# Kernel optimization log

Measured on AMD Instinct MI355X. Metric: run time of the kernel, lower is better.

Reference implementation:

```python
import jax, jax.numpy as jnp
import numpy as np
from jax import lax

T, H, K, V, O = 8192, 2048, 512, 512, 2048


def setup_inputs() -> dict:
    key = jax.random.key(0)
    ks = jax.random.split(key, 11)
    s_h = 1.0 / np.sqrt(H)
    s_v = 1.0 / np.sqrt(V)
    return {
        "hidden_state": jax.random.normal(ks[0], (T, H), jnp.float32),
        "Wq": jax.random.normal(ks[1], (H, K), jnp.float32) * s_h,
        "bq": jax.random.normal(ks[2], (K,), jnp.float32) * 0.02,
        "Wk": jax.random.normal(ks[3], (H, K), jnp.float32) * s_h,
        "bk": jax.random.normal(ks[4], (K,), jnp.float32) * 0.02,
        "Wv": jax.random.normal(ks[5], (H, V), jnp.float32) * s_h,
        "bv": jax.random.normal(ks[6], (V,), jnp.float32) * 0.02,
        "Wg": jax.random.normal(ks[7], (H, K), jnp.float32) * s_h,
        "bg": jax.random.normal(ks[8], (K,), jnp.float32) * 0.02,
        "Wo": jax.random.normal(ks[9], (V, O), jnp.float32) * s_v,
        "bo": jax.random.normal(ks[10], (O,), jnp.float32) * 0.02,
    }


def reference(hidden_state, Wq, bq, Wk, bk, Wv, bv, Wg, bg, Wo, bo):
    # Batched projections (torch Linear: x @ W^T + b; here W stored as [in,out])
    q = hidden_state @ Wq + bq                    # [T, K]
    k = jax.nn.sigmoid(hidden_state @ Wk + bk)    # [T, K]
    g = jax.nn.sigmoid(hidden_state @ Wg + bg)    # [T, K]
    v = hidden_state @ Wv + bv                    # [T, V]

    def step(state, qkvg):
        qi, ki, vi, gi = qkvg
        # state: [K, V]; gated decay per key-dim row, then outer-product write
        state = state * gi[:, None] + ki[:, None] * vi[None, :]
        out_i = qi @ state  # == state.T @ qi -> [V]
        return state, out_i

    init = jnp.zeros((K, V), hidden_state.dtype)
    final_state, outs = lax.scan(step, init, (q, k, v, g))  # outs: [T, V]
    output = outs @ Wo + bo                                  # [T, O]
    return output, final_state
```

## Files before the change

### kernel.cpp

```cpp
#include <hip/hip_runtime.h>

#define T_LEN 8192
#define H_DIM 2048
#define K_DIM 512
#define V_DIM 512
#define O_DIM 2048
#define CHUNK 64
#define NCHUNK 128

typedef short bf16x8 __attribute__((ext_vector_type(8)));
typedef float f32x4 __attribute__((ext_vector_type(4)));

typedef const __attribute__((address_space(1))) void* gptr1_t;
typedef __attribute__((address_space(3))) void* lptr3_t;

__device__ __forceinline__ float b2f(unsigned short u) {
    unsigned int i = ((unsigned int)u) << 16;
    float f;
    __builtin_memcpy(&f, &i, 4);
    return f;
}
__device__ __forceinline__ unsigned short f2b(float f) {
    unsigned int i;
    __builtin_memcpy(&i, &f, 4);
    unsigned int r = (i + 0x7FFFu + ((i >> 16) & 1u)) >> 16;
    return (unsigned short)r;
}
__device__ __forceinline__ float fw(float v) {
    return fminf(fmaxf(v, -1e30f), 1e30f);
}

#define BARX() asm volatile("s_barrier" ::: "memory")
#define ORDER() asm volatile("" ::: "memory")

#define GLDS(gp, dstByte)                                                      \
    __builtin_amdgcn_global_load_lds((gptr1_t)(const void*)(gp),               \
                                     (lptr3_t)(void*)((char*)lds + (dstByte)), \
                                     16, 0, 0)
#define STAGE2(p0, p1, dstBase)                                                \
    do {                                                                       \
        GLDS(p0, (dstBase) + tid * 16);                                        \
        GLDS(p1, (dstBase) + 8192 + tid * 16);                                 \
    } while (0)

__global__ __launch_bounds__(256) void prep_k(const float* __restrict__ hs,
                                              unsigned short* __restrict__ hsb,
                                              const float* __restrict__ Wq,
                                              const float* __restrict__ Wk,
                                              const float* __restrict__ Wg,
                                              const float* __restrict__ Wv,
                                              const float* __restrict__ Wo,
                                              unsigned short* __restrict__ WT,
                                              unsigned short* __restrict__ WoT,
                                              int* __restrict__ flag) {
    __shared__ unsigned short tile[32][33];
    long bid = blockIdx.x;
    int tid = threadIdx.x;
    if (bid < 8192) {
        long i = (bid * 256 + tid) * 8;
        unsigned int wd[4];
#pragma unroll
        for (int u = 0; u < 4; u++) {
            unsigned short lo = f2b(hs[i + 2 * u]);
            unsigned short hi = f2b(hs[i + 2 * u + 1]);
            wd[u] = (unsigned int)lo | ((unsigned int)hi << 16);
        }
        uint4 pk; pk.x = wd[0]; pk.y = wd[1]; pk.z = wd[2]; pk.w = wd[3];
        *(uint4*)(hsb + i) = pk;
        return;
    }
    if (bid == 8192 + 5 * 1024) {
        unsigned short* As = &tile[0][0];
        unsigned short* Bs = &tile[0][0] + 512;
        for (int idx = tid; idx < 512; idx += 256) {
            int r = idx >> 5, c = idx & 31;
            float av = (c == 0) ? (float)(r + 1) : (c == 1 ? 1.0f : 0.0f);
            float bv = (c == 0) ? 1.0f : (c == 1 ? (float)(1024 * (r + 1)) : 0.0f);
            As[idx] = f2b(av);
            Bs[idx] = f2b(bv);
        }
        __syncthreads();
        if (tid < 64) {
            int ln15 = tid & 15, q4 = tid >> 4;
            bf16x8 a = *(const bf16x8*)(As + ln15 * 32 + q4 * 8);
            bf16x8 b = *(const bf16x8*)(Bs + ln15 * 32 + q4 * 8);
            f32x4 acc = {0.f, 0.f, 0.f, 0.f};
            acc = __builtin_amdgcn_mfma_f32_16x16x32_bf16(a, b, acc, 0, 0, 0);
            bool h0 = true, h1 = true;
#pragma unroll
            for (int i = 0; i < 4; i++) {
                float e0 = (float)((q4 * 4 + i + 1) + 1024 * (ln15 + 1));
                float e1 = (float)((ln15 + 1) + 1024 * (q4 * 4 + i + 1));
                h0 = h0 && (acc[i] == e0);
                h1 = h1 && (acc[i] == e1);
            }
            unsigned long long b0 = __ballot(h0 ? 1 : 0);
            unsigned long long b1 = __ballot(h1 ? 1 : 0);
            if (tid == 0) *flag = (b0 == ~0ull) ? 0 : ((b1 == ~0ull) ? 1 : 0);
        }
        return;
    }
    int t = (int)(bid - 8192);
    int mat = t >> 10, tl = t & 1023;
    const float* in; unsigned short* outp; int R, C, br, bc;
    if (mat < 4) {
        in = mat == 0 ? Wq : mat == 1 ? Wk : mat == 2 ? Wg : Wv;
        outp = WT + (long)mat * 512 * H_DIM;
        R = H_DIM; C = 512; br = tl >> 4; bc = tl & 15;
    } else {
        in = Wo; outp = WoT; R = V_DIM; C = O_DIM; br = tl & 15; bc = tl >> 4;
    }
    int tc = tid & 31, tr = tid >> 5;
#pragma unroll
    for (int i = 0; i < 4; i++) {
        int r = tr + 8 * i;
        long idx = (long)(br * 32 + r) * C + bc * 32 + tc;
        tile[r][tc] = f2b(in[idx]);
    }
    __syncthreads();
#pragma unroll
    for (int i = 0; i < 4; i++) {
        int r = tr + 8 * i;
        outp[(long)(bc * 32 + r) * R + br * 32 + tc] = tile[tc][r];
    }
}

__global__ __launch_bounds__(512, 2) void proj_gemm256_k(const unsigned short* __restrict__ A,
                                                         const unsigned short* __restrict__ WT,
                                                         const float* __restrict__ bq,
                                                         const float* __restrict__ bk,
                                                         const float* __restrict__ bg,
                                                         const float* __restrict__ bv,
                                                         unsigned short* __restrict__ qb,
                                                         unsigned short* __restrict__ kb,
                                                         float* __restrict__ gb,
                                                         unsigned short* __restrict__ vT,
                                                         const int* __restrict__ flagp) {
    __shared__ short lds[65536];
    int fl = *flagp;
    int tid = threadIdx.x;
    int lane = tid & 63;
    int ln15 = lane & 15, q4 = lane >> 4;
    int w = tid >> 6;
    int wm = w >> 2, wn = w & 3;
    long m0 = (long)blockIdx.x * 256, n0 = (long)blockIdx.y * 256;

    unsigned slot = ((unsigned)(q4 * 16)) ^ ((unsigned)((ln15 & 7) << 4));
    unsigned aoff0 = (unsigned)(wm * 8192 + ln15 * 128) + slot;
    unsigned boff0 = 65536u + (unsigned)(wn * 4096 + ln15 * 128) + slot;

    int idx0 = tid, idx1 = 512 + tid;
    int r0_ = idx0 >> 3, r1_ = idx1 >> 3;
    int c80 = (idx0 & 7) ^ (r0_ & 7);
    int c81 = (idx1 & 7) ^ (r1_ & 7);
    int trA0 = ((r0_ >> 6) & 1) * 128 + (r0_ & 63);
    int trA1 = ((r1_ >> 6) & 1) * 128 + (r1_ & 63);
    int tcB0 = ((r0_ >> 5) & 3) * 64 + (r0_ & 31);
    int tcB1 = ((r1_ >> 5) & 3) * 64 + (r1_ & 31);
    const unsigned short* pAlo0 = A + (m0 + trA0) * (long)H_DIM + c80 * 8;
    const unsigned short* pAlo1 = A + (m0 + trA1) * (long)H_DIM + c81 * 8;
    const unsigned short* pAhi0 = pAlo0 + 64 * H_DIM;
    const unsigned short* pAhi1 = pAlo1 + 64 * H_DIM;
    const unsigned short* pBlo0 = WT + (n0 + tcB0) * (long)H_DIM + c80 * 8;
    const unsigned short* pBlo1 = WT + (n0 + tcB1) * (long)H_DIM + c81 * 8;
    const unsigned short* pBhi0 = pBlo0 + 32 * H_DIM;
    const unsigned short* pBhi1 = pBlo1 + 32 * H_DIM;

    f32x4 acc[8][4] = {};

    STAGE2(pAlo0, pAlo1, 0);
    STAGE2(pBlo0, pBlo1, 65536);
    ORDER();
    STAGE2(pBhi0, pBhi1, 65536 + 16384);
    STAGE2(pAhi0, pAhi1, 16384);
    ORDER();
    pAlo0 += 64; pAlo1 += 64; pBlo0 += 64; pBlo1 += 64;
    STAGE2(pAlo0, pAlo1, 32768);
    STAGE2(pBlo0, pBlo1, 65536 + 32768);
    ORDER();
    pAlo0 += 64; pAlo1 += 64; pBlo0 += 64; pBlo1 += 64;
    pAhi0 += 64; pAhi1 += 64; pBhi0 += 64; pBhi1 += 64;
    asm volatile("s_waitcnt vmcnt(8)" ::: "memory");
    BARX();

    int cur = 0;
    const char* L = (const char*)lds;
    for (int kt = 0; kt < H_DIM; kt += 64, cur ^= 1) {
        int nxt = cur ^ 1;
        unsigned bufb = (unsigned)cur << 15;
        unsigned ab0 = aoff0 + bufb, ab1 = ab0 ^ 64u;
        unsigned bb0 = boff0 + bufb, bb1 = bb0 ^ 64u;
        bf16x8 af[4][2], blo[2][2], bhi[2][2];

#pragma unroll
        for (int i = 0; i < 4; i++) {
            af[i][0] = *(const bf16x8*)(L + ab0 + i * 2048);
            af[i][1] = *(const bf16x8*)(L + ab1 + i * 2048);
        }
#pragma unroll
        for (int j = 0; j < 2; j++) {
            blo[j][0] = *(const bf16x8*)(L + bb0 + j * 2048);
            blo[j][1] = *(const bf16x8*)(L + bb1 + j * 2048);
        }
        STAGE2(pBhi0, pBhi1, 65536 + nxt * 32768 + 16384);
        __builtin_amdgcn_s_setprio(1);
#pragma unroll
        for (int i = 0; i < 4; i++)
#pragma unroll
            for (int j = 0; j < 2; j++) {
                acc[i][j] = __builtin_amdgcn_mfma_f32_16x16x32_bf16(af[i][0], blo[j][0], acc[i][j], 0, 0, 0);
                acc[i][j] = __builtin_amdgcn_mfma_f32_16x16x32_bf16(af[i][1], blo[j][1], acc[i][j], 0, 0, 0);
            }
        __builtin_amdgcn_s_setprio(0);
        asm volatile("s_waitcnt vmcnt(8)" ::: "memory");
        BARX();

#pragma unroll
        for (int j = 0; j < 2; j++) {
            bhi[j][0] = *(const bf16x8*)(L + bb0 + 16384 + j * 2048);
            bhi[j][1] = *(const bf16x8*)(L + bb1 + 16384 + j * 2048);
        }
        STAGE2(pAhi0, pAhi1, nxt * 32768 + 16384);
        __builtin_amdgcn_s_setprio(1);
#pragma unroll
        for (int i = 0; i < 4; i++)
#pragma unroll
            for (int j = 0; j < 2; j++) {
                acc[i][2 + j] = __builtin_amdgcn_mfma_f32_16x16x32_bf16(af[i][0], bhi[j][0], acc[i][2 + j], 0, 0, 0);
                acc[i][2 + j] = __builtin_amdgcn_mfma_f32_16x16x32_bf16(af[i][1], bhi[j][1], acc[i][2 + j], 0, 0, 0);
            }
        __builtin_amdgcn_s_setprio(0);
        asm volatile("s_waitcnt vmcnt(8)" ::: "memory");
        BARX();

#pragma unroll
        for (int i = 0; i < 4; i++) {
            af[i][0] = *(const bf16x8*)(L + ab0 + 16384 + i * 2048);
            af[i][1] = *(const bf16x8*)(L + ab1 + 16384 + i * 2048);
        }
        STAGE2(pAlo0, pAlo1, cur * 32768);
        __builtin_amdgcn_s_setprio(1);
#pragma unroll
        for (int i = 0; i < 4; i++)
#pragma unroll
            for (int j = 0; j < 2; j++) {
                acc[4 + i][2 + j] = __builtin_amdgcn_mfma_f32_16x16x32_bf16(af[i][0], bhi[j][0], acc[4 + i][2 + j], 0, 0, 0);
                acc[4 + i][2 + j] = __builtin_amdgcn_mfma_f32_16x16x32_bf16(af[i][1], bhi[j][1], acc[4 + i][2 + j], 0, 0, 0);
            }
        __builtin_amdgcn_s_setprio(0);

        STAGE2(pBlo0, pBlo1, 65536 + cur * 32768);
        __builtin_amdgcn_s_setprio(1);
#pragma unroll
        for (int i = 0; i < 4; i++)
#pragma unroll
            for (int j = 0; j < 2; j++) {
                acc[4 + i][j] = __builtin_amdgcn_mfma_f32_16x16x32_bf16(af[i][0], blo[j][0], acc[4 + i][j], 0, 0, 0);
                acc[4 + i][j] = __builtin_amdgcn_mfma_f32_16x16x32_bf16(af[i][1], blo[j][1], acc[4 + i][j], 0, 0, 0);
            }
        __builtin_amdgcn_s_setprio(0);
        asm volatile("s_waitcnt vmcnt(8)" ::: "memory");
        BARX();

        pAlo0 += 64; pAlo1 += 64; pAhi0 += 64; pAhi1 += 64;
        pBlo0 += 64; pBlo1 += 64; pBhi0 += 64; pBhi1 += 64;
    }

    int seg = (int)(n0 >> 9);
    int nl0 = (int)(n0 & 511);
    const float* bias = seg == 0 ? bq : seg == 1 ? bk : seg == 2 ? bg : bv;

    if (seg == 3 && fl == 0) {
#pragma unroll
        for (int im = 0; im < 8; im++)
#pragma unroll
            for (int jn = 0; jn < 4; jn++) {
                int nl = nl0 + wn * 64 + (jn >> 1) * 32 + (jn & 1) * 16 + ln15;
                float bsv = bias[nl];
                long mb = m0 + wm * 128 + (im >> 2) * 64 + (im & 3) * 16 + q4 * 4;
                unsigned short h0 = f2b(fw(acc[im][jn][0] + bsv));
                unsigned short h1 = f2b(fw(acc[im][jn][1] + bsv));
                unsigned short h2 = f2b(fw(acc[im][jn][2] + bsv));
                unsigned short h3 = f2b(fw(acc[im][jn][3] + bsv));
                uint2 pk;
                pk.x = (unsigned int)h0 | ((unsigned int)h1 << 16);
                pk.y = (unsigned int)h2 | ((unsigned int)h3 << 16);
                *(uint2*)(vT + (long)nl * T_LEN + mb) = pk;
            }
    } else {
#pragma unroll
        for (int im = 0; im < 8; im++)
#pragma unroll
            for (int jn = 0; jn < 4; jn++)
#pragma unroll
                for (int ii = 0; ii < 4; ii++) {
                    int dm = fl ? ln15 : q4 * 4 + ii;
                    int dn = fl ? q4 * 4 + ii : ln15;
                    long m = m0 + wm * 128 + (im >> 2) * 64 + (im & 3) * 16 + dm;
                    int nl = nl0 + wn * 64 + (jn >> 1) * 32 + (jn & 1) * 16 + dn;
                    float v = fw(acc[im][jn][ii] + bias[nl]);
                    if (seg == 1 || seg == 2) v = 1.0f / (1.0f + __expf(-v));
                    if (seg == 0)
                        qb[m * K_DIM + nl] = f2b(v);
                    else if (seg == 1)
                        kb[m * K_DIM + nl] = f2b(v);
                    else if (seg == 2)
                        gb[m * K_DIM + nl] = v;
                    else
                        vT[(long)nl * T_LEN + m] = f2b(v);
                }
    }
}

__global__ __launch_bounds__(512, 2) void gemm256_k(const unsigned short* __restrict__ A,
                                                    const unsigned short* __restrict__ BT,
                                                    const float* __restrict__ bias,
                                                    float* __restrict__ out,
                                                    int N, int KT,
                                                    const int* __restrict__ flagp) {
    __shared__ short lds[65536];
    int fl = *flagp;
    int tid = threadIdx.x;
    int lane = tid & 63;
    int ln15 = lane & 15, q4 = lane >> 4;
    int w = tid >> 6;
    int wm = w >> 2, wn = w & 3;
    long m0 = (long)blockIdx.x * 256, n0 = (long)blockIdx.y * 256;

    unsigned slot = ((unsigned)(q4 * 16)) ^ ((unsigned)((ln15 & 7) << 4));
    unsigned aoff0 = (unsigned)(wm * 8192 + ln15 * 128) + slot;
    unsigned boff0 = 65536u + (unsigned)(wn * 4096 + ln15 * 128) + slot;

    int idx0 = tid, idx1 = 512 + tid;
    int r0_ = idx0 >> 3, r1_ = idx1 >> 3;
    int c80 = (idx0 & 7) ^ (r0_ & 7);
    int c81 = (idx1 & 7) ^ (r1_ & 7);
    int trA0 = ((r0_ >> 6) & 1) * 128 + (r0_ & 63);
    int trA1 = ((r1_ >> 6) & 1) * 128 + (r1_ & 63);
    int tcB0 = ((r0_ >> 5) & 3) * 64 + (r0_ & 31);
    int tcB1 = ((r1_ >> 5) & 3) * 64 + (r1_ & 31);
    const unsigned short* pAlo0 = A + (m0 + trA0) * (long)KT + c80 * 8;
    const unsigned short* pAlo1 = A + (m0 + trA1) * (long)KT + c81 * 8;
    const unsigned short* pAhi0 = pAlo0 + 64 * KT;
    const unsigned short* pAhi1 = pAlo1 + 64 * KT;
    const unsigned short* pBlo0 = BT + (n0 + tcB0) * (long)KT + c80 * 8;
    const unsigned short* pBlo1 = BT + (n0 + tcB1) * (long)KT + c81 * 8;
    const unsigned short* pBhi0 = pBlo0 + 32 * KT;
    const unsigned short* pBhi1 = pBlo1 + 32 * KT;

    f32x4 acc[8][4] = {};

    STAGE2(pAlo0, pAlo1, 0);
    STAGE2(pBlo0, pBlo1, 65536);
    ORDER();
    STAGE2(pBhi0, pBhi1, 65536 + 16384);
    STAGE2(pAhi0, pAhi1, 16384);
    ORDER();
    pAlo0 += 64; pAlo1 += 64; pBlo0 += 64; pBlo1 += 64;
    STAGE2(pAlo0, pAlo1, 32768);
    STAGE2(pBlo0, pBlo1, 65536 + 32768);
    ORDER();
    pAlo0 += 64; pAlo1 += 64; pBlo0 += 64; pBlo1 += 64;
    pAhi0 += 64; pAhi1 += 64; pBhi0 += 64; pBhi1 += 64;
    asm volatile("s_waitcnt vmcnt(8)" ::: "memory");
    BARX();

    int cur = 0;
    const char* L = (const char*)lds;
    for (int kt = 0; kt < KT; kt += 64, cur ^= 1) {
        int nxt = cur ^ 1;
        unsigned bufb = (unsigned)cur << 15;
        unsigned ab0 = aoff0 + bufb, ab1 = ab0 ^ 64u;
        unsigned bb0 = boff0 + bufb, bb1 = bb0 ^ 64u;
        bf16x8 af[4][2], blo[2][2], bhi[2][2];

#pragma unroll
        for (int i = 0; i < 4; i++) {
            af[i][0] = *(const bf16x8*)(L + ab0 + i * 2048);
            af[i][1] = *(const bf16x8*)(L + ab1 + i * 2048);
        }
#pragma unroll
        for (int j = 0; j < 2; j++) {
            blo[j][0] = *(const bf16x8*)(L + bb0 + j * 2048);
            blo[j][1] = *(const bf16x8*)(L + bb1 + j * 2048);
        }
        STAGE2(pBhi0, pBhi1, 65536 + nxt * 32768 + 16384);
        __builtin_amdgcn_s_setprio(1);
#pragma unroll
        for (int i = 0; i < 4; i++)
#pragma unroll
            for (int j = 0; j < 2; j++) {
                acc[i][j] = __builtin_amdgcn_mfma_f32_16x16x32_bf16(af[i][0], blo[j][0], acc[i][j], 0, 0, 0);
                acc[i][j] = __builtin_amdgcn_mfma_f32_16x16x32_bf16(af[i][1], blo[j][1], acc[i][j], 0, 0, 0);
            }
        __builtin_amdgcn_s_setprio(0);
        asm volatile("s_waitcnt vmcnt(8)" ::: "memory");
        BARX();

#pragma unroll
        for (int j = 0; j < 2; j++) {
            bhi[j][0] = *(const bf16x8*)(L + bb0 + 16384 + j * 2048);
            bhi[j][1] = *(const bf16x8*)(L + bb1 + 16384 + j * 2048);
        }
        STAGE2(pAhi0, pAhi1, nxt * 32768 + 16384);
        __builtin_amdgcn_s_setprio(1);
#pragma unroll
        for (int i = 0; i < 4; i++)
#pragma unroll
            for (int j = 0; j < 2; j++) {
                acc[i][2 + j] = __builtin_amdgcn_mfma_f32_16x16x32_bf16(af[i][0], bhi[j][0], acc[i][2 + j], 0, 0, 0);
                acc[i][2 + j] = __builtin_amdgcn_mfma_f32_16x16x32_bf16(af[i][1], bhi[j][1], acc[i][2 + j], 0, 0, 0);
            }
        __builtin_amdgcn_s_setprio(0);
        asm volatile("s_waitcnt vmcnt(8)" ::: "memory");
        BARX();

#pragma unroll
        for (int i = 0; i < 4; i++) {
            af[i][0] = *(const bf16x8*)(L + ab0 + 16384 + i * 2048);
            af[i][1] = *(const bf16x8*)(L + ab1 + 16384 + i * 2048);
        }
        STAGE2(pAlo0, pAlo1, cur * 32768);
        __builtin_amdgcn_s_setprio(1);
#pragma unroll
        for (int i = 0; i < 4; i++)
#pragma unroll
            for (int j = 0; j < 2; j++) {
                acc[4 + i][2 + j] = __builtin_amdgcn_mfma_f32_16x16x32_bf16(af[i][0], bhi[j][0], acc[4 + i][2 + j], 0, 0, 0);
                acc[4 + i][2 + j] = __builtin_amdgcn_mfma_f32_16x16x32_bf16(af[i][1], bhi[j][1], acc[4 + i][2 + j], 0, 0, 0);
            }
        __builtin_amdgcn_s_setprio(0);

        STAGE2(pBlo0, pBlo1, 65536 + cur * 32768);
        __builtin_amdgcn_s_setprio(1);
#pragma unroll
        for (int i = 0; i < 4; i++)
#pragma unroll
            for (int j = 0; j < 2; j++) {
                acc[4 + i][j] = __builtin_amdgcn_mfma_f32_16x16x32_bf16(af[i][0], blo[j][0], acc[4 + i][j], 0, 0, 0);
                acc[4 + i][j] = __builtin_amdgcn_mfma_f32_16x16x32_bf16(af[i][1], blo[j][1], acc[4 + i][j], 0, 0, 0);
            }
        __builtin_amdgcn_s_setprio(0);
        asm volatile("s_waitcnt vmcnt(8)" ::: "memory");
        BARX();

        pAlo0 += 64; pAlo1 += 64; pAhi0 += 64; pAhi1 += 64;
        pBlo0 += 64; pBlo1 += 64; pBhi0 += 64; pBhi1 += 64;
    }

#pragma unroll
    for (int im = 0; im < 8; im++)
#pragma unroll
        for (int jn = 0; jn < 4; jn++)
#pragma unroll
            for (int ii = 0; ii < 4; ii++) {
                int dm = fl ? ln15 : q4 * 4 + ii;
                int dn = fl ? q4 * 4 + ii : ln15;
                long m = m0 + wm * 128 + (im >> 2) * 64 + (im & 3) * 16 + dm;
                long n = n0 + wn * 64 + (jn >> 1) * 32 + (jn & 1) * 16 + dn;
                out[m * N + n] = fw(acc[im][jn][ii] + bias[n]);
            }
}

__global__ __launch_bounds__(256) void cumprod_k(const float* __restrict__ g,
                                                 unsigned short* __restrict__ q,
                                                 unsigned short* __restrict__ k,
                                                 unsigned short* __restrict__ khatT,
                                                 float* __restrict__ pend) {
    __shared__ unsigned short tile[256][80];
    int c = blockIdx.x;
    int half = blockIdx.y;
    int tid = threadIdx.x;
    int d = half * 256 + tid;
    long base = (long)c * CHUNK * K_DIM + d;
    float gv[CHUNK];
#pragma unroll
    for (int s = 0; s < CHUNK; s++) gv[s] = g[base + (long)s * K_DIM];
    float P = 1.0f;
#pragma unroll
    for (int s = 0; s < CHUNK; s++) { P = fmaxf(P * gv[s], 1e-37f); gv[s] = P; }
    pend[c * K_DIM + d] = P;
    float Pend = P;
#pragma unroll
    for (int s8 = 0; s8 < CHUNK; s8 += 8) {
        unsigned int packed[4];
#pragma unroll
        for (int u = 0; u < 8; u++) {
            int s = s8 + u;
            long idx = base + (long)s * K_DIM;
            float Pc = gv[s];
            float qv = fw(b2f(q[idx]) * Pc);
            q[idx] = f2b(qv);
            float kv = b2f(k[idx]);
            float kt = kv / Pc;
            kt = fmaxf(fminf(kt, 3e37f), -3e37f);
            k[idx] = f2b(kt);
            float ratio = Pend / Pc;
            unsigned short kh = f2b(fw(kv * ratio));
            if (u & 1)
                packed[u >> 1] |= ((unsigned int)kh) << 16;
            else
                packed[u >> 1] = kh;
        }
        uint4 pk;
        pk.x = packed[0]; pk.y = packed[1]; pk.z = packed[2]; pk.w = packed[3];
        *(uint4*)&tile[tid][s8] = pk;
    }
    __syncthreads();
    int wv = tid >> 6, l = tid & 63;
    int colb = (l & 7) * 8;
#pragma unroll
    for (int j = 0; j < 8; j++) {
        int row = wv * 64 + j * 8 + (l >> 3);
        uint4 pk = *(const uint4*)&tile[row][colb];
        *(uint4*)(khatT + (long)(half * 256 + row) * T_LEN + c * CHUNK + colb) = pk;
    }
}

__global__ __launch_bounds__(256) void scan_k(const unsigned short* __restrict__ khatT,
                                              const unsigned short* __restrict__ vT,
                                              const float* __restrict__ pend,
                                              unsigned short* __restrict__ ST,
                                              float* __restrict__ fstate,
                                              const int* __restrict__ flagp) {
    int fl = *flagp;
    int lane = threadIdx.x & 63, w = threadIdx.x >> 6;
    int ln15 = lane & 15, q4 = lane >> 4;
    int k0 = (blockIdx.x & 15) * 32 + (w & 1) * 16;
    int v0 = (blockIdx.x >> 4) * 32 + (w >> 1) * 16;
    f32x4 acc = {0.f, 0.f, 0.f, 0.f};
    const unsigned short* kb_ = khatT + (long)(k0 + ln15) * T_LEN + q4 * 8;
    const unsigned short* vb_ = vT + (long)(v0 + ln15) * T_LEN + q4 * 8;

    bf16x8 kf0[2], vf0[2], kf1[2], vf1[2], kf2[2], vf2[2], kf3[2], vf3[2];
    float4 pdv[4];
    float pds[4];

#define LOADSET(s, c)                                                        \
    do {                                                                     \
        long off_ = (long)(c) * CHUNK;                                       \
        kf##s[0] = *(const bf16x8*)(kb_ + off_);                             \
        kf##s[1] = *(const bf16x8*)(kb_ + off_ + 32);                        \
        vf##s[0] = *(const bf16x8*)(vb_ + off_);                             \
        vf##s[1] = *(const bf16x8*)(vb_ + off_ + 32);                        \
        if (!fl)                                                             \
            pdv[s] = *(const float4*)(pend + (c) * K_DIM + k0 + q4 * 4);     \
        else                                                                 \
            pds[s] = pend[(c) * K_DIM + k0 + ln15];                          \
    } while (0)

    LOADSET(0, 0); LOADSET(1, 1); LOADSET(2, 2); LOADSET(3, 3);

#define STEP(s, c)                                                                             \
    do {                                                                                       \
        if (!fl) {                                                                             \
            uint2 pk_;                                                                         \
            pk_.x = (unsigned int)f2b(fw(acc[0])) | ((unsigned int)f2b(fw(acc[1])) << 16);     \
            pk_.y = (unsigned int)f2b(fw(acc[2])) | ((unsigned int)f2b(fw(acc[3])) << 16);     \
            *(uint2*)(ST + ((long)(c) * V_DIM + v0 + ln15) * K_DIM + k0 + q4 * 4) = pk_;       \
            acc[0] *= pdv[s].x; acc[1] *= pdv[s].y; acc[2] *= pdv[s].z; acc[3] *= pdv[s].w;    \
        } else {                                                                               \
            ST[((long)(c) * V_DIM + v0 + q4 * 4 + 0) * K_DIM + k0 + ln15] = f2b(fw(acc[0]));   \
            ST[((long)(c) * V_DIM + v0 + q4 * 4 + 1) * K_DIM + k0 + ln15] = f2b(fw(acc[1]));   \
            ST[((long)(c) * V_DIM + v0 + q4 * 4 + 2) * K_DIM + k0 + ln15] = f2b(fw(acc[2]));   \
            ST[((long)(c) * V_DIM + v0 + q4 * 4 + 3) * K_DIM + k0 + ln15] = f2b(fw(acc[3]));   \
            acc[0] *= pds[s]; acc[1] *= pds[s]; acc[2] *= pds[s]; acc[3] *= pds[s];            \
        }                                                                                      \
        acc = __builtin_amdgcn_mfma_f32_16x16x32_bf16(kf##s[0], vf##s[0], acc, 0, 0, 0);       \
        acc = __builtin_amdgcn_mfma_f32_16x16x32_bf16(kf##s[1], vf##s[1], acc, 0, 0, 0);       \
        int cp_ = (c) + 4;                                                                     \
        if (cp_ > NCHUNK - 1) cp_ = NCHUNK - 1;                                                \
        LOADSET(s, cp_);                                                                       \
    } while (0)

    for (int c = 0; c < NCHUNK; c += 4) {
        STEP(0, c);
        STEP(1, c + 1);
        STEP(2, c + 2);
        STEP(3, c + 3);
    }
#undef STEP
#undef LOADSET

#pragma unroll
    for (int i = 0; i < 4; i++) {
        int dk = fl ? ln15 : q4 * 4 + i;
        int dv = fl ? q4 * 4 + i : ln15;
        fstate[(long)(k0 + dk) * V_DIM + v0 + dv] = fw(acc[i]);
    }
}

__global__ __launch_bounds__(256) void intra_k(const unsigned short* __restrict__ qs,
                                               const unsigned short* __restrict__ ks,
                                               const unsigned short* __restrict__ vT,
                                               const unsigned short* __restrict__ ST,
                                               unsigned short* __restrict__ outs,
                                               const int* __restrict__ flagp) {
    __shared__ unsigned short Ab[64 * 72];
    int fl = *flagp;
    long cloc = blockIdx.x >> 2;
    int c = (int)cloc, h = blockIdx.x & 3;
    int lane = threadIdx.x & 63, w = threadIdx.x >> 6;
    int ln15 = lane & 15, q4 = lane >> 4;
    long t0 = (long)c * CHUNK;

    {
        f32x4 accA[4] = {};
        for (int kk = 0; kk < K_DIM; kk += 32) {
            bf16x8 a = *(const bf16x8*)(qs + (t0 + 16 * w + ln15) * K_DIM + kk + q4 * 8);
#pragma unroll
            for (int j = 0; j < 4; j++) {
                bf16x8 b = *(const bf16x8*)(ks + (t0 + 16 * j + ln15) * K_DIM + kk + q4 * 8);
                accA[j] = __builtin_amdgcn_mfma_f32_16x16x32_bf16(a, b, accA[j], 0, 0, 0);
            }
        }
#pragma unroll
        for (int j = 0; j < 4; j++)
#pragma unroll
            for (int i = 0; i < 4; i++) {
                int dt = fl ? ln15 : q4 * 4 + i;
                int ds = fl ? q4 * 4 + i : ln15;
                int tl = 16 * w + dt;
                int s = 16 * j + ds;
                float av = (s <= tl) ? accA[j][i] : 0.0f;
                Ab[tl * 72 + s] = f2b(fw(av));
            }
    }
    __syncthreads();

    int v0 = h * 128 + w * 32;
    f32x4 acc[4][2] = {};
    for (int kk = 0; kk < K_DIM; kk += 32) {
        bf16x8 a[4], b[2];
#pragma unroll
        for (int i = 0; i < 4; i++)
            a[i] = *(const bf16x8*)(qs + (t0 + 16 * i + ln15) * K_DIM + kk + q4 * 8);
#pragma unroll
        for (int j = 0; j < 2; j++)
            b[j] = *(const bf16x8*)(ST + (cloc * V_DIM + v0 + 16 * j + ln15) * K_DIM + kk + q4 * 8);
#pragma unroll
        for (int i = 0; i < 4; i++)
#pragma unroll
            for (int j = 0; j < 2; j++)
                acc[i][j] = __builtin_amdgcn_mfma_f32_16x16x32_bf16(a[i], b[j], acc[i][j], 0, 0, 0);
    }
#pragma unroll
    for (int s0 = 0; s0 < CHUNK; s0 += 32) {
        bf16x8 a[4], b[2];
#pragma unroll
        for (int i = 0; i < 4; i++)
            a[i] = *(const bf16x8*)(Ab + (16 * i + ln15) * 72 + s0 + q4 * 8);
#pragma unroll
        for (int j = 0; j < 2; j++)
            b[j] = *(const bf16x8*)(vT + (long)(v0 + 16 * j + ln15) * T_LEN + t0 + s0 + q4 * 8);
#pragma unroll
        for (int i = 0; i < 4; i++)
#pragma unroll
            for (int j = 0; j < 2; j++)
                acc[i][j] = __builtin_amdgcn_mfma_f32_16x16x32_bf16(a[i], b[j], acc[i][j], 0, 0, 0);
    }
#pragma unroll
    for (int i = 0; i < 4; i++)
#pragma unroll
        for (int j = 0; j < 2; j++)
#pragma unroll
            for (int ii = 0; ii < 4; ii++) {
                int dt = fl ? ln15 : q4 * 4 + ii;
                int dv = fl ? q4 * 4 + ii : ln15;
                outs[(t0 + 16 * i + dt) * V_DIM + v0 + 16 * j + dv] = f2b(fw(acc[i][j][ii]));
            }
}

extern "C" void kernel_launch(void* const* d_in, const int* in_sizes, int n_in,
                              void* d_out, int out_size, void* d_ws, size_t ws_size,
                              hipStream_t stream) {
    const float* hs = (const float*)d_in[0];
    const float* Wq = (const float*)d_in[1];
    const float* bq = (const float*)d_in[2];
    const float* Wk = (const float*)d_in[3];
    const float* bk = (const float*)d_in[4];
    const float* Wv = (const float*)d_in[5];
    const float* bv = (const float*)d_in[6];
    const float* Wg = (const float*)d_in[7];
    const float* bg = (const float*)d_in[8];
    const float* Wo = (const float*)d_in[9];
    const float* bo = (const float*)d_in[10];

    float* out = (float*)d_out;

    char* ws = (char*)d_ws;
    const size_t MB = 1024 * 1024;
    unsigned short* WT = (unsigned short*)(ws + 0 * MB);
    unsigned short* outsb = (unsigned short*)(ws + 0 * MB);
    unsigned short* WoT = (unsigned short*)(ws + 8 * MB);
    unsigned short* qb = (unsigned short*)(ws + 10 * MB);
    unsigned short* kb = (unsigned short*)(ws + 18 * MB);
    unsigned short* vTb = (unsigned short*)(ws + 26 * MB);
    unsigned short* khatT = (unsigned short*)(ws + 34 * MB);
    float* pend = (float*)(ws + 42 * MB);
    int* flags = (int*)(ws + 42 * MB + 256 * 1024);
    float* gb = (float*)(ws + 44 * MB);
    unsigned short* STb = (unsigned short*)(ws + 44 * MB);
    unsigned short* hsb = (unsigned short*)(ws + 60 * MB);
    float* fsspare = (float*)(ws + 108 * MB);
    (void)ws_size; (void)in_sizes; (void)n_in;

    float* finalst =
        ((long)out_size >= (long)T_LEN * O_DIM + (long)K_DIM * V_DIM)
            ? out + (long)T_LEN * O_DIM
            : fsspare;

    dim3 b256(256);
    prep_k<<<dim3(8192 + 5 * 1024 + 1), b256, 0, stream>>>(hs, hsb, Wq, Wk, Wg, Wv, Wo, WT, WoT,
                                                           flags);
    proj_gemm256_k<<<dim3(T_LEN / 256, 8), dim3(512), 0, stream>>>(
        hsb, WT, bq, bk, bg, bv, qb, kb, gb, vTb, flags);
    cumprod_k<<<dim3(NCHUNK, K_DIM / 256), b256, 0, stream>>>(gb, qb, kb, khatT, pend);
    scan_k<<<dim3(256), b256, 0, stream>>>(khatT, vTb, pend, STb, finalst, flags);
    intra_k<<<dim3(4 * NCHUNK), b256, 0, stream>>>(qb, kb, vTb, STb, outsb, flags);
    gemm256_k<<<dim3(T_LEN / 256, O_DIM / 256), dim3(512), 0, stream>>>(
        outsb, WoT, bo, out, O_DIM, V_DIM, flags);
}
```

Measured before the change: 397.1 us.

## Split chunk-state scan into parallel group scans with carry propagation and fixup

The sequential inter-chunk state scan, previously 256 blocks walking all 128 chunks, becomes 8 independent groups of 16 chunks run in parallel. A carry kernel combines the group-end states with the cumulative decay products to form each group's incoming carry and the final state, and a fixup kernel adds the decayed carry into the bf16 chunk states. This aims to shorten the serial critical path and raise occupancy, at the cost of extra passes over the state buffer and an extra bf16 rounding. intra_k is also retiled so each block covers 256 value columns instead of 128, halving its grid size.

```diff
diff --git a/kernel.cpp b/kernel.cpp
--- a/kernel.cpp
+++ b/kernel.cpp
@@ -7,6 +7,8 @@
 #define O_DIM 2048
 #define CHUNK 64
 #define NCHUNK 128
+#define GRP 16
+#define NGRP 8
 
 typedef short bf16x8 __attribute__((ext_vector_type(8)));
 typedef float f32x4 __attribute__((ext_vector_type(4)));
@@ -517,17 +519,21 @@
     }
 }
 
-__global__ __launch_bounds__(256) void scan_k(const unsigned short* __restrict__ khatT,
-                                              const unsigned short* __restrict__ vT,
-                                              const float* __restrict__ pend,
-                                              unsigned short* __restrict__ ST,
-                                              float* __restrict__ fstate,
-                                              const int* __restrict__ flagp) {
+__global__ __launch_bounds__(256) void scan_local_k(const unsigned short* __restrict__ khatT,
+                                                    const unsigned short* __restrict__ vT,
+                                                    const float* __restrict__ pend,
+                                                    unsigned short* __restrict__ ST,
+                                                    float* __restrict__ Lend,
+                                                    const int* __restrict__ flagp) {
     int fl = *flagp;
+    int bid = blockIdx.x;
+    int g = bid >> 8;
+    int t8 = bid & 255;
     int lane = threadIdx.x & 63, w = threadIdx.x >> 6;
     int ln15 = lane & 15, q4 = lane >> 4;
-    int k0 = (blockIdx.x & 15) * 32 + (w & 1) * 16;
-    int v0 = (blockIdx.x >> 4) * 32 + (w >> 1) * 16;
+    int k0 = (t8 & 15) * 32 + (w & 1) * 16;
+    int v0 = (t8 >> 4) * 32 + (w >> 1) * 16;
+    int c0 = g * GRP, cn = c0 + GRP;
     f32x4 acc = {0.f, 0.f, 0.f, 0.f};
     const unsigned short* kb_ = khatT + (long)(k0 + ln15) * T_LEN + q4 * 8;
     const unsigned short* vb_ = vT + (long)(v0 + ln15) * T_LEN + q4 * 8;
@@ -549,7 +555,7 @@
             pds[s] = pend[(c) * K_DIM + k0 + ln15];                          \
     } while (0)
 
-    LOADSET(0, 0); LOADSET(1, 1); LOADSET(2, 2); LOADSET(3, 3);
+    LOADSET(0, c0); LOADSET(1, c0 + 1); LOADSET(2, c0 + 2); LOADSET(3, c0 + 3);
 
 #define STEP(s, c)                                                                             \
     do {                                                                                       \
@@ -569,11 +575,11 @@
         acc = __builtin_amdgcn_mfma_f32_16x16x32_bf16(kf##s[0], vf##s[0], acc, 0, 0, 0);       \
         acc = __builtin_amdgcn_mfma_f32_16x16x32_bf16(kf##s[1], vf##s[1], acc, 0, 0, 0);       \
         int cp_ = (c) + 4;                                                                     \
-        if (cp_ > NCHUNK - 1) cp_ = NCHUNK - 1;                                                \
+        if (cp_ > cn - 1) cp_ = cn - 1;                                                        \
         LOADSET(s, cp_);                                                                       \
     } while (0)
 
-    for (int c = 0; c < NCHUNK; c += 4) {
+    for (int c = c0; c < cn; c += 4) {
         STEP(0, c);
         STEP(1, c + 1);
         STEP(2, c + 2);
@@ -582,12 +588,85 @@
 #undef STEP
 #undef LOADSET
 
-#pragma unroll
-    for (int i = 0; i < 4; i++) {
-        int dk = fl ? ln15 : q4 * 4 + i;
-        int dv = fl ? q4 * 4 + i : ln15;
-        fstate[(long)(k0 + dk) * V_DIM + v0 + dv] = fw(acc[i]);
-    }
+    float* Lg = Lend + (long)g * K_DIM * V_DIM;
+    if (!fl) {
+        float4 o;
+        o.x = fw(acc[0]); o.y = fw(acc[1]); o.z = fw(acc[2]); o.w = fw(acc[3]);
+        *(float4*)(Lg + (long)(v0 + ln15) * K_DIM + k0 + q4 * 4) = o;
+    } else {
+#pragma unroll
+        for (int i = 0; i < 4; i++)
+            Lg[(long)(v0 + q4 * 4 + i) * K_DIM + k0 + ln15] = fw(acc[i]);
+    }
+}
+
+__global__ __launch_bounds__(256) void carry_k(const float* __restrict__ Lend,
+                                               const float* __restrict__ pend,
+                                               float* __restrict__ CarryT,
+                                               float* __restrict__ Dloc,
+                                               float* __restrict__ fstate) {
+    int bid = blockIdx.x, tid = threadIdx.x;
+    if (bid < 256) {
+        int linear = bid * 256 + tid;
+        int v = linear >> 7;
+        int k4 = (linear & 127) * 4;
+        float cx = 0.f, cy = 0.f, cz = 0.f, cw = 0.f;
+#pragma unroll
+        for (int g = 0; g < NGRP; g++) {
+            float4 o; o.x = cx; o.y = cy; o.z = cz; o.w = cw;
+            *(float4*)(CarryT + (long)g * K_DIM * V_DIM + (long)v * K_DIM + k4) = o;
+            float4 le = *(const float4*)(Lend + (long)g * K_DIM * V_DIM + (long)v * K_DIM + k4);
+            float dx = 1.f, dy = 1.f, dz = 1.f, dw = 1.f;
+#pragma unroll
+            for (int j = 0; j < GRP; j++) {
+                float4 p = *(const float4*)(pend + (g * GRP + j) * K_DIM + k4);
+                dx *= p.x; dy *= p.y; dz *= p.z; dw *= p.w;
+            }
+            cx = fw(le.x + dx * cx);
+            cy = fw(le.y + dy * cy);
+            cz = fw(le.z + dz * cz);
+            cw = fw(le.w + dw * cw);
+        }
+        fstate[(long)(k4 + 0) * V_DIM + v] = cx;
+        fstate[(long)(k4 + 1) * V_DIM + v] = cy;
+        fstate[(long)(k4 + 2) * V_DIM + v] = cz;
+        fstate[(long)(k4 + 3) * V_DIM + v] = cw;
+    } else {
+        int idx = (bid - 256) * 256 + tid;
+        int g = idx >> 9;
+        int k = idx & 511;
+        float run = 1.f;
+#pragma unroll
+        for (int j = 0; j < GRP; j++) {
+            Dloc[(g * GRP + j) * K_DIM + k] = run;
+            run *= pend[(g * GRP + j) * K_DIM + k];
+        }
+    }
+}
+
+__global__ __launch_bounds__(256) void fixup_k(unsigned short* __restrict__ ST,
+                                               const float* __restrict__ Dloc,
+                                               const float* __restrict__ CarryT,
+                                               const int* __restrict__ flagp) {
+    (void)flagp;
+    int bid = blockIdx.x;
+    int c = GRP + (bid >> 8);
+    int inner = (bid & 255) * 256 + threadIdx.x;
+    int v = inner >> 7;
+    int k4 = (inner & 127) * 4;
+    int g = c >> 4;
+    unsigned short* stp = ST + ((long)c * V_DIM + v) * K_DIM + k4;
+    uint2 st = *(const uint2*)stp;
+    float4 dl = *(const float4*)(Dloc + c * K_DIM + k4);
+    float4 cr = *(const float4*)(CarryT + (long)g * K_DIM * V_DIM + (long)v * K_DIM + k4);
+    unsigned short o0 = f2b(fw(b2f((unsigned short)(st.x & 0xFFFF)) + dl.x * cr.x));
+    unsigned short o1 = f2b(fw(b2f((unsigned short)(st.x >> 16)) + dl.y * cr.y));
+    unsigned short o2 = f2b(fw(b2f((unsigned short)(st.y & 0xFFFF)) + dl.z * cr.z));
+    unsigned short o3 = f2b(fw(b2f((unsigned short)(st.y >> 16)) + dl.w * cr.w));
+    uint2 ot;
+    ot.x = (unsigned int)o0 | ((unsigned int)o1 << 16);
+    ot.y = (unsigned int)o2 | ((unsigned int)o3 << 16);
+    *(uint2*)stp = ot;
 }
 
 __global__ __launch_bounds__(256) void intra_k(const unsigned short* __restrict__ qs,
@@ -598,8 +677,8 @@
                                                const int* __restrict__ flagp) {
     __shared__ unsigned short Ab[64 * 72];
     int fl = *flagp;
-    long cloc = blockIdx.x >> 2;
-    int c = (int)cloc, h = blockIdx.x & 3;
+    long cloc = blockIdx.x >> 1;
+    int c = (int)cloc, h = blockIdx.x & 1;
     int lane = threadIdx.x & 63, w = threadIdx.x >> 6;
     int ln15 = lane & 15, q4 = lane >> 4;
     long t0 = (long)c * CHUNK;
@@ -628,41 +707,41 @@
     }
     __syncthreads();
 
-    int v0 = h * 128 + w * 32;
-    f32x4 acc[4][2] = {};
+    int v0 = h * 256 + w * 64;
+    f32x4 acc[4][4] = {};
     for (int kk = 0; kk < K_DIM; kk += 32) {
-        bf16x8 a[4], b[2];
+        bf16x8 a[4], b[4];
 #pragma unroll
         for (int i = 0; i < 4; i++)
             a[i] = *(const bf16x8*)(qs + (t0 + 16 * i + ln15) * K_DIM + kk + q4 * 8);
 #pragma unroll
-        for (int j = 0; j < 2; j++)
+        for (int j = 0; j < 4; j++)
             b[j] = *(const bf16x8*)(ST + (cloc * V_DIM + v0 + 16 * j + ln15) * K_DIM + kk + q4 * 8);
 #pragma unroll
         for (int i = 0; i < 4; i++)
 #pragma unroll
-            for (int j = 0; j < 2; j++)
+            for (int j = 0; j < 4; j++)
                 acc[i][j] = __builtin_amdgcn_mfma_f32_16x16x32_bf16(a[i], b[j], acc[i][j], 0, 0, 0);
     }
 #pragma unroll
     for (int s0 = 0; s0 < CHUNK; s0 += 32) {
-        bf16x8 a[4], b[2];
+        bf16x8 a[4], b[4];
 #pragma unroll
         for (int i = 0; i < 4; i++)
             a[i] = *(const bf16x8*)(Ab + (16 * i + ln15) * 72 + s0 + q4 * 8);
 #pragma unroll
-        for (int j = 0; j < 2; j++)
+        for (int j = 0; j < 4; j++)
             b[j] = *(const bf16x8*)(vT + (long)(v0 + 16 * j + ln15) * T_LEN + t0 + s0 + q4 * 8);
 #pragma unroll
         for (int i = 0; i < 4; i++)
 #pragma unroll
-            for (int j = 0; j < 2; j++)
+            for (int j = 0; j < 4; j++)
                 acc[i][j] = __builtin_amdgcn_mfma_f32_16x16x32_bf16(a[i], b[j], acc[i][j], 0, 0, 0);
     }
 #pragma unroll
     for (int i = 0; i < 4; i++)
 #pragma unroll
-        for (int j = 0; j < 2; j++)
+        for (int j = 0; j < 4; j++)
 #pragma unroll
             for (int ii = 0; ii < 4; ii++) {
                 int dt = fl ? ln15 : q4 * 4 + ii;
@@ -691,18 +770,21 @@
     char* ws = (char*)d_ws;
     const size_t MB = 1024 * 1024;
     unsigned short* WT = (unsigned short*)(ws + 0 * MB);
+    float* Lendb = (float*)(ws + 0 * MB);
     unsigned short* outsb = (unsigned short*)(ws + 0 * MB);
     unsigned short* WoT = (unsigned short*)(ws + 8 * MB);
     unsigned short* qb = (unsigned short*)(ws + 10 * MB);
     unsigned short* kb = (unsigned short*)(ws + 18 * MB);
     unsigned short* vTb = (unsigned short*)(ws + 26 * MB);
     unsigned short* khatT = (unsigned short*)(ws + 34 * MB);
+    float* CarryT = (float*)(ws + 34 * MB);
     float* pend = (float*)(ws + 42 * MB);
     int* flags = (int*)(ws + 42 * MB + 256 * 1024);
-    float* gb = (float*)(ws + 44 * MB);
+    float* Dloc = (float*)(ws + 42 * MB + 512 * 1024);
+    float* fsspare = (float*)(ws + 43 * MB);
+    float* gbuf = (float*)(ws + 44 * MB);
     unsigned short* STb = (unsigned short*)(ws + 44 * MB);
     unsigned short* hsb = (unsigned short*)(ws + 60 * MB);
-    float* fsspare = (float*)(ws + 108 * MB);
     (void)ws_size; (void)in_sizes; (void)n_in;
 
     float* finalst =
@@ -714,10 +796,12 @@
     prep_k<<<dim3(8192 + 5 * 1024 + 1), b256, 0, stream>>>(hs, hsb, Wq, Wk, Wg, Wv, Wo, WT, WoT,
                                                            flags);
     proj_gemm256_k<<<dim3(T_LEN / 256, 8), dim3(512), 0, stream>>>(
-        hsb, WT, bq, bk, bg, bv, qb, kb, gb, vTb, flags);
-    cumprod_k<<<dim3(NCHUNK, K_DIM / 256), b256, 0, stream>>>(gb, qb, kb, khatT, pend);
-    scan_k<<<dim3(256), b256, 0, stream>>>(khatT, vTb, pend, STb, finalst, flags);
-    intra_k<<<dim3(4 * NCHUNK), b256, 0, stream>>>(qb, kb, vTb, STb, outsb, flags);
+        hsb, WT, bq, bk, bg, bv, qb, kb, gbuf, vTb, flags);
+    cumprod_k<<<dim3(NCHUNK, K_DIM / 256), b256, 0, stream>>>(gbuf, qb, kb, khatT, pend);
+    scan_local_k<<<dim3(NGRP * 256), b256, 0, stream>>>(khatT, vTb, pend, STb, Lendb, flags);
+    carry_k<<<dim3(272), b256, 0, stream>>>(Lendb, pend, CarryT, Dloc, finalst);
+    fixup_k<<<dim3((NCHUNK - GRP) * 256), b256, 0, stream>>>(STb, Dloc, CarryT, flags);
+    intra_k<<<dim3(2 * NCHUNK), b256, 0, stream>>>(qb, kb, vTb, STb, outsb, flags);
     gemm256_k<<<dim3(T_LEN / 256, O_DIM / 256), dim3(512), 0, stream>>>(
         outsb, WoT, bo, out, O_DIM, V_DIM, flags);
 }
```

Result: slower. 415.0 us (+4.5%).
